# Kernel optimization log

Measured on AMD Instinct MI355X. Metric: run time of the kernel, lower is better.

Reference implementation:

```python
import jax, jax.numpy as jnp
import numpy as np

N_NODES = 50000
N_EDGES = 800000
IN_DIM = 512
HIDDEN = 512
HEADS = 4                       # num_heads // 2 per direction
C_HEAD = HIDDEN // (2 * HEADS)  # 64 -> each direction outputs HIDDEN//2
NEG_SLOPE = 0.2                 # PyG GATConv default leaky_relu slope
BN_EPS = 1e-5


def gat_conv(x, src, dst, W, att_src, att_dst, bias):
    """PyG-style GATConv, concat=True. Edge (src -> dst), aggregated at dst.
    x:[N,D] W:[D,H,C] att_*:[H,C] bias:[H*C] -> [N,H*C]."""
    N = x.shape[0]
    h = jnp.einsum('nd,dhc->nhc', x, W)              # [N,H,C]
    a_s = jnp.sum(h * att_src, axis=-1)              # [N,H]
    a_d = jnp.sum(h * att_dst, axis=-1)              # [N,H]
    e = jax.nn.leaky_relu(a_s[src] + a_d[dst], NEG_SLOPE)   # [E,H]
    m = jax.ops.segment_max(e, dst, num_segments=N)         # [N,H]
    m = jnp.where(jnp.isfinite(m), m, 0.0)
    ex = jnp.exp(e - m[dst])                                # [E,H]
    denom = jax.ops.segment_sum(ex, dst, num_segments=N)    # [N,H]
    alpha = ex / (denom[dst] + 1e-16)                       # [E,H]
    out = jax.ops.segment_sum(alpha[:, :, None] * h[src], dst, num_segments=N)
    return out.reshape(N, HEADS * C_HEAD) + bias


def setup_inputs() -> dict:
    key = jax.random.key(0)
    ks = jax.random.split(key, 12)
    glorot = lambda k, shape, fan: (jax.random.normal(k, shape, jnp.float32)
                                    * np.sqrt(2.0 / fan))
    inp = {
        'x': jax.random.normal(ks[0], (N_NODES, IN_DIM), jnp.float32),
        'edge_index': jax.random.randint(ks[1], (2, N_EDGES), 0, N_NODES,
                                         dtype=jnp.int32).astype(jnp.int64),
        # forward-direction GATConv params
        'W_f': glorot(ks[2], (IN_DIM, HEADS, C_HEAD), IN_DIM),
        'att_src_f': glorot(ks[3], (HEADS, C_HEAD), C_HEAD),
        'att_dst_f': glorot(ks[4], (HEADS, C_HEAD), C_HEAD),
        'bias_f': jnp.zeros((HEADS * C_HEAD,), jnp.float32),
        # backward-direction GATConv params
        'W_b': glorot(ks[5], (IN_DIM, HEADS, C_HEAD), IN_DIM),
        'att_src_b': glorot(ks[6], (HEADS, C_HEAD), C_HEAD),
        'att_dst_b': glorot(ks[7], (HEADS, C_HEAD), C_HEAD),
        'bias_b': jnp.zeros((HEADS * C_HEAD,), jnp.float32),
        # fusion linear + batchnorm
        'W_fuse': glorot(ks[8], (HIDDEN, HIDDEN), HIDDEN),
        'b_fuse': jnp.zeros((HIDDEN,), jnp.float32),
        'bn_gamma': jnp.ones((HIDDEN,), jnp.float32),
        'bn_beta': jnp.zeros((HIDDEN,), jnp.float32),
    }
    return inp


def reference(x, edge_index, W_f, att_src_f, att_dst_f, bias_f,
              W_b, att_src_b, att_dst_b, bias_b,
              W_fuse, b_fuse, bn_gamma, bn_beta):
    src, dst = edge_index[0], edge_index[1]
    fwd = gat_conv(x, src, dst, W_f, att_src_f, att_dst_f, bias_f)
    # reversed edges: torch.flip(edge_index, [0]) swaps src/dst rows
    bwd = gat_conv(x, dst, src, W_b, att_src_b, att_dst_b, bias_b)
    combined = jnp.concatenate([fwd, bwd], axis=1)          # [N, HIDDEN]
    fused = combined @ W_fuse + b_fuse
    mean = jnp.mean(fused, axis=0)
    var = jnp.mean(jnp.square(fused - mean), axis=0)        # biased, as BN uses
    normed = (fused - mean) * jax.lax.rsqrt(var + BN_EPS) * bn_gamma + bn_beta
    return jax.nn.relu(normed)
```

## Files before the change

### kernel.cpp

```cpp
#include <hip/hip_runtime.h>
#include <math.h>

#define HEADS 4
#define CH 64
#define HC 256
#define HID 512
#define KDIM 512

typedef __attribute__((ext_vector_type(8))) short short8;
typedef __attribute__((ext_vector_type(4))) float f32x4;

__device__ __forceinline__ float lrelu(float x){ return x > 0.f ? x : 0.2f*x; }

__device__ __forceinline__ unsigned short f2bf(float f){
  unsigned u = __float_as_uint(f);
  unsigned r = (u + 0x7FFFu + ((u >> 16) & 1u)) >> 16;
  return (unsigned short)r;
}
__device__ __forceinline__ float bf2f(unsigned short u){
  return __uint_as_float(((unsigned)u) << 16);
}

__global__ void k_zero(int* cntD, int* cntS, float* gsum, float* gsq, int N){
  int i = blockIdx.x*blockDim.x + threadIdx.x;
  int stride = gridDim.x*blockDim.x;
  for(int j=i; j<N; j+=stride){ cntD[j]=0; cntS[j]=0; }
  if(i < HID){ gsum[i]=0.f; gsq[i]=0.f; }
}

__global__ void k_detect(const int* __restrict__ ei32, int* flag){
  __shared__ int any;
  if(threadIdx.x==0) any = 0;
  __syncthreads();
  int v = 0;
  for(int i=threadIdx.x; i<1024; i+=blockDim.x) v |= ei32[2*i+1];
  if(v) atomicOr(&any, 1);
  __syncthreads();
  if(threadIdx.x==0) *flag = (any==0) ? 1 : 0;
}

__global__ void k_convert(const int* __restrict__ ei32, const int* __restrict__ flag,
                          int* __restrict__ src, int* __restrict__ dst, int E){
  int i = blockIdx.x*blockDim.x + threadIdx.x;
  if(i>=E) return;
  if(*flag){ src[i] = ei32[2*i];  dst[i] = ei32[2*(E+i)]; }
  else     { src[i] = ei32[i];    dst[i] = ei32[E+i];     }
}

__global__ void k_cvt_x(const float4* __restrict__ in4, uint2* __restrict__ out2, long n4){
  long i = (long)blockIdx.x*blockDim.x + threadIdx.x;
  long stride = (long)gridDim.x*blockDim.x;
  for(long j=i; j<n4; j+=stride){
    float4 v = in4[j];
    uint2 o;
    o.x = (unsigned)f2bf(v.x) | ((unsigned)f2bf(v.y) << 16);
    o.y = (unsigned)f2bf(v.z) | ((unsigned)f2bf(v.w) << 16);
    out2[j] = o;
  }
}

__global__ void k_transcvt(const float* __restrict__ src, unsigned short* __restrict__ dst,
                           int K, int C){
  int i = blockIdx.x*blockDim.x + threadIdx.x;
  if(i >= C*K) return;
  int n = i / K;
  int k = i - n*K;
  dst[(size_t)n*K + k] = f2bf(src[(size_t)k*C + n]);
}

__global__ __launch_bounds__(256) void k_gemm_mfma(
    const unsigned short* __restrict__ A,
    const unsigned short* __restrict__ Bt,
    float* __restrict__ Cf, unsigned short* __restrict__ Cb,
    int M, int Nc, int K, const float* __restrict__ bias){
  __shared__ __align__(16) unsigned short Asm[128*32];
  __shared__ __align__(16) unsigned short Bsm[128*32];
  int tid = threadIdx.x;
  int w = tid >> 6, lane = tid & 63;
  int wr = (w >> 1) * 64, wc = (w & 1) * 64;
  int lcol = lane & 15, lkb = lane >> 4;
  int row0 = blockIdx.y * 128, col0 = blockIdx.x * 128;

  int c0 = tid, c1 = tid + 256;
  int ar0 = c0 >> 2, ak0 = (c0 & 3) * 8;
  int ar1 = c1 >> 2, ak1 = (c1 & 3) * 8;

  f32x4 acc[4][4] = {};

  for(int kt = 0; kt < K; kt += 32){
    short8 va0 = *(const short8*)(A  + (size_t)(row0 + ar0)*K + kt + ak0);
    short8 va1 = *(const short8*)(A  + (size_t)(row0 + ar1)*K + kt + ak1);
    short8 vb0 = *(const short8*)(Bt + (size_t)(col0 + ar0)*K + kt + ak0);
    short8 vb1 = *(const short8*)(Bt + (size_t)(col0 + ar1)*K + kt + ak1);
    __syncthreads();
    *(short8*)(Asm + ar0*32 + ak0) = va0;
    *(short8*)(Asm + ar1*32 + ak1) = va1;
    *(short8*)(Bsm + ar0*32 + ak0) = vb0;
    *(short8*)(Bsm + ar1*32 + ak1) = vb1;
    __syncthreads();

    short8 af[4], bfr[4];
    #pragma unroll
    for(int mi=0; mi<4; mi++)
      af[mi] = *(const short8*)(Asm + (wr + mi*16 + lcol)*32 + lkb*8);
    #pragma unroll
    for(int ni=0; ni<4; ni++)
      bfr[ni] = *(const short8*)(Bsm + (wc + ni*16 + lcol)*32 + lkb*8);
    #pragma unroll
    for(int mi=0; mi<4; mi++)
      #pragma unroll
      for(int ni=0; ni<4; ni++)
        acc[mi][ni] = __builtin_amdgcn_mfma_f32_16x16x32_bf16(af[mi], bfr[ni], acc[mi][ni], 0, 0, 0);
  }

  int lr = (lane >> 4) * 4;
  #pragma unroll
  for(int mi=0; mi<4; mi++){
    int gr0 = row0 + wr + mi*16 + lr;
    #pragma unroll
    for(int ni=0; ni<4; ni++){
      int gc = col0 + wc + ni*16 + lcol;
      float bv = bias ? bias[gc] : 0.f;
      #pragma unroll
      for(int r=0; r<4; r++){
        int gr = gr0 + r;
        if(gr < M){
          float v = acc[mi][ni][r] + bv;
          if(Cb) Cb[(size_t)gr*Nc + gc] = f2bf(v);
          else   Cf[(size_t)gr*Nc + gc] = v;
        }
      }
    }
  }
}

__global__ __launch_bounds__(256) void k_att(
    const unsigned short* __restrict__ h,
    const float* __restrict__ att_sf, const float* __restrict__ att_df,
    const float* __restrict__ att_sb, const float* __restrict__ att_db,
    float4* __restrict__ asf, float4* __restrict__ adf,
    float4* __restrict__ asb, float4* __restrict__ adb, int N){
  int w = (blockIdx.x*(blockDim.x>>6)) + (threadIdx.x>>6);
  int lane = threadIdx.x & 63;
  if(w >= N) return;
  float psf[4], pdf_[4], psb[4], pdb_[4];
  #pragma unroll
  for(int i=0;i<4;i++){
    float vf = bf2f(h[(size_t)w*HID + i*64 + lane]);
    float vb = bf2f(h[(size_t)w*HID + 256 + i*64 + lane]);
    psf[i]  = vf*att_sf[i*64+lane];  pdf_[i] = vf*att_df[i*64+lane];
    psb[i]  = vb*att_sb[i*64+lane];  pdb_[i] = vb*att_db[i*64+lane];
  }
  #pragma unroll
  for(int off=32; off; off>>=1){
    #pragma unroll
    for(int i=0;i<4;i++){
      psf[i]  += __shfl_xor(psf[i],  off);
      pdf_[i] += __shfl_xor(pdf_[i], off);
      psb[i]  += __shfl_xor(psb[i],  off);
      pdb_[i] += __shfl_xor(pdb_[i], off);
    }
  }
  if(lane==0){
    asf[w] = make_float4(psf[0],psf[1],psf[2],psf[3]);
    adf[w] = make_float4(pdf_[0],pdf_[1],pdf_[2],pdf_[3]);
    asb[w] = make_float4(psb[0],psb[1],psb[2],psb[3]);
    adb[w] = make_float4(pdb_[0],pdb_[1],pdb_[2],pdb_[3]);
  }
}

__global__ void k_edge(const int* __restrict__ src, const int* __restrict__ dst,
    const float4* __restrict__ asf, const float4* __restrict__ adf,
    const float4* __restrict__ asb, const float4* __restrict__ adb,
    float4* __restrict__ ef, float4* __restrict__ eb,
    int* __restrict__ cntD, int* __restrict__ cntS, int E){
  int e = blockIdx.x*blockDim.x + threadIdx.x;
  if(e>=E) return;
  int s = src[e], d = dst[e];
  float4 a = asf[s], b = adf[d], r;
  r.x = lrelu(a.x+b.x); r.y = lrelu(a.y+b.y); r.z = lrelu(a.z+b.z); r.w = lrelu(a.w+b.w);
  ef[e] = r;
  a = asb[d]; b = adb[s];
  r.x = lrelu(a.x+b.x); r.y = lrelu(a.y+b.y); r.z = lrelu(a.z+b.z); r.w = lrelu(a.w+b.w);
  eb[e] = r;
  atomicAdd(&cntD[d], 1);
  atomicAdd(&cntS[s], 1);
}

__global__ __launch_bounds__(1024) void k_scan_local(
    const int* __restrict__ cntD, const int* __restrict__ cntS,
    int* __restrict__ rsD, int* __restrict__ curD,
    int* __restrict__ rsS, int* __restrict__ curS,
    int* __restrict__ bsums, int n, int nb){
  const int* cnt = blockIdx.y ? cntS : cntD;
  int* rs  = blockIdx.y ? rsS  : rsD;
  int* cur = blockIdx.y ? curS : curD;
  int* bs  = bsums + blockIdx.y*nb;
  __shared__ int sh[1024];
  int i = blockIdx.x*1024 + threadIdx.x;
  int v = (i<n) ? cnt[i] : 0;
  sh[threadIdx.x] = v;
  __syncthreads();
  for(int off=1; off<1024; off<<=1){
    int t = (threadIdx.x>=off) ? sh[threadIdx.x-off] : 0;
    __syncthreads();
    sh[threadIdx.x] += t;
    __syncthreads();
  }
  if(i<n){ int e0 = sh[threadIdx.x] - v; rs[i] = e0; cur[i] = e0; }
  if(threadIdx.x==1023) bs[blockIdx.x] = sh[1023];
}

__global__ __launch_bounds__(256) void k_scan_bsums(int* __restrict__ bsums,
                                                    int* __restrict__ totals, int nb){
  int* bs = bsums + blockIdx.x*nb;
  __shared__ int sh[256];
  int v = (threadIdx.x < nb) ? bs[threadIdx.x] : 0;
  sh[threadIdx.x] = v;
  __syncthreads();
  for(int off=1; off<256; off<<=1){
    int t = (threadIdx.x>=off) ? sh[threadIdx.x-off] : 0;
    __syncthreads();
    sh[threadIdx.x] += t;
    __syncthreads();
  }
  if(threadIdx.x < nb) bs[threadIdx.x] = sh[threadIdx.x] - v;
  if(threadIdx.x == 255) totals[blockIdx.x] = sh[255];
}

__global__ __launch_bounds__(1024) void k_scan_add(
    int* __restrict__ rsD, int* __restrict__ curD,
    int* __restrict__ rsS, int* __restrict__ curS,
    const int* __restrict__ bsums, const int* __restrict__ totals, int n, int nb){
  const int* bs = bsums + blockIdx.y*nb;
  int* rs  = blockIdx.y ? rsS  : rsD;
  int* cur = blockIdx.y ? curS : curD;
  int add = bs[blockIdx.x];
  int i = blockIdx.x*1024 + threadIdx.x;
  if(i<n){ rs[i] += add; cur[i] += add; }
  if(i==0) rs[n] = totals[blockIdx.y];
}

__global__ void k_scatter(const int* __restrict__ src, const int* __restrict__ dst,
    int* __restrict__ curD, int* __restrict__ curS,
    int* __restrict__ listD, int* __restrict__ listS, int E){
  int e = blockIdx.x*blockDim.x + threadIdx.x;
  if(e>=E) return;
  int p = atomicAdd(&curD[dst[e]], 1);  listD[p] = e;
  int q = atomicAdd(&curS[src[e]], 1);  listS[q] = e;
}

__global__ __launch_bounds__(256) void k_agg(
    const int* __restrict__ rs, const int* __restrict__ list,
    const float4* __restrict__ etab, const int* __restrict__ gidx,
    const unsigned short* __restrict__ h, int hoff, const float* __restrict__ bias,
    unsigned short* __restrict__ combined, int N, int out_off){
  int w = (blockIdx.x*(blockDim.x>>6)) + (threadIdx.x>>6);
  int lane = threadIdx.x & 63;
  if(w >= N) return;
  int beg = rs[w], end = rs[w+1];
  float4 m = make_float4(-1e30f,-1e30f,-1e30f,-1e30f);
  for(int j=beg+lane; j<end; j+=64){
    float4 ev = etab[list[j]];
    m.x = fmaxf(m.x, ev.x); m.y = fmaxf(m.y, ev.y);
    m.z = fmaxf(m.z, ev.z); m.w = fmaxf(m.w, ev.w);
  }
  #pragma unroll
  for(int off=32; off; off>>=1){
    m.x = fmaxf(m.x, __shfl_xor(m.x, off));
    m.y = fmaxf(m.y, __shfl_xor(m.y, off));
    m.z = fmaxf(m.z, __shfl_xor(m.z, off));
    m.w = fmaxf(m.w, __shfl_xor(m.w, off));
  }
  float4 acc = make_float4(0,0,0,0);
  float4 den = make_float4(0,0,0,0);
  for(int j=beg; j<end; j++){
    int e = list[j];
    float4 ev = etab[e];
    int g = gidx[e];
    const unsigned short* hp = h + (size_t)g*HID + hoff;
    float e0 = __expf(ev.x - m.x), e1 = __expf(ev.y - m.y);
    float e2 = __expf(ev.z - m.z), e3 = __expf(ev.w - m.w);
    den.x += e0; den.y += e1; den.z += e2; den.w += e3;
    acc.x += e0 * bf2f(hp[lane]);
    acc.y += e1 * bf2f(hp[64+lane]);
    acc.z += e2 * bf2f(hp[128+lane]);
    acc.w += e3 * bf2f(hp[192+lane]);
  }
  unsigned short* co = combined + (size_t)w*HID + out_off;
  co[lane]     = f2bf(acc.x/(den.x+1e-16f) + bias[lane]);
  co[64+lane]  = f2bf(acc.y/(den.y+1e-16f) + bias[64+lane]);
  co[128+lane] = f2bf(acc.z/(den.z+1e-16f) + bias[128+lane]);
  co[192+lane] = f2bf(acc.w/(den.w+1e-16f) + bias[192+lane]);
}

__global__ __launch_bounds__(512) void k_bn_stats(const unsigned short* __restrict__ fused, int N,
                                                  float* __restrict__ gsum, float* __restrict__ gsq){
  int c = threadIdx.x;
  int rows_per = (N + gridDim.x - 1) / gridDim.x;
  int r0 = blockIdx.x * rows_per;
  int r1 = min(N, r0 + rows_per);
  float s = 0.f, q = 0.f;
  for(int r=r0; r<r1; r++){
    float v = bf2f(fused[(size_t)r*HID + c]);
    s += v; q += v*v;
  }
  atomicAdd(&gsum[c], s);
  atomicAdd(&gsq[c], q);
}

__global__ __launch_bounds__(512) void k_bn_final(const float* __restrict__ gsum, const float* __restrict__ gsq,
    const float* __restrict__ gamma, const float* __restrict__ beta,
    float* __restrict__ scale, float* __restrict__ shift, int N){
  int c = threadIdx.x;
  float mean = gsum[c] / (float)N;
  float var  = gsq[c] / (float)N - mean*mean;
  float sc = gamma[c] * rsqrtf(var + 1e-5f);
  scale[c] = sc;
  shift[c] = beta[c] - mean*sc;
}

__global__ void k_bn_apply(const uint2* __restrict__ fused2, const float4* __restrict__ scale4,
                           const float4* __restrict__ shift4, float4* __restrict__ out4, long n4){
  long i = (long)blockIdx.x*blockDim.x + threadIdx.x;
  long stride = (long)gridDim.x*blockDim.x;
  for(long j=i; j<n4; j+=stride){
    uint2 u = fused2[j];
    int c4 = (int)(j & 127);
    float4 sc = scale4[c4], sh = shift4[c4];
    float4 r;
    r.x = fmaxf(__uint_as_float(u.x << 16)          * sc.x + sh.x, 0.f);
    r.y = fmaxf(__uint_as_float(u.x & 0xffff0000u)  * sc.y + sh.y, 0.f);
    r.z = fmaxf(__uint_as_float(u.y << 16)          * sc.z + sh.z, 0.f);
    r.w = fmaxf(__uint_as_float(u.y & 0xffff0000u)  * sc.w + sh.w, 0.f);
    out4[j] = r;
  }
}

extern "C" void kernel_launch(void* const* d_in, const int* in_sizes, int n_in,
                              void* d_out, int out_size, void* d_ws, size_t ws_size,
                              hipStream_t stream){
  const float* x        = (const float*)d_in[0];
  const int*   ei32     = (const int*)  d_in[1];
  const float* W_f      = (const float*)d_in[2];
  const float* att_sf   = (const float*)d_in[3];
  const float* att_df   = (const float*)d_in[4];
  const float* bias_f   = (const float*)d_in[5];
  const float* W_b      = (const float*)d_in[6];
  const float* att_sb   = (const float*)d_in[7];
  const float* att_db   = (const float*)d_in[8];
  const float* bias_b   = (const float*)d_in[9];
  const float* W_fuse   = (const float*)d_in[10];
  const float* b_fuse   = (const float*)d_in[11];
  const float* bn_gamma = (const float*)d_in[12];
  const float* bn_beta  = (const float*)d_in[13];

  const int N = in_sizes[0] / 512;
  const int E = in_sizes[1] / 2;
  const int Mp = ((N + 127) / 128) * 128;
  const int nb = (N + 1023) / 1024;

  char* ws = (char*)d_ws;
  size_t off = 0;
  auto alloc = [&](size_t bytes)->char*{
    char* p = ws + off;
    off = (off + bytes + 255) & ~(size_t)255;
    return p;
  };

  int*   srcI   = (int*)  alloc((size_t)E*4);
  int*   dstI   = (int*)  alloc((size_t)E*4);
  unsigned short* xb      = (unsigned short*)alloc((size_t)Mp*KDIM*2);
  unsigned short* Wcat_t  = (unsigned short*)alloc((size_t)HID*KDIM*2);
  unsigned short* Wfuse_t = (unsigned short*)alloc((size_t)HID*KDIM*2);
  unsigned short* h       = (unsigned short*)alloc((size_t)Mp*HID*2);
  float4* asf   = (float4*)alloc((size_t)N*16);
  float4* adf   = (float4*)alloc((size_t)N*16);
  float4* asb   = (float4*)alloc((size_t)N*16);
  float4* adb   = (float4*)alloc((size_t)N*16);
  float4* e_f   = (float4*)alloc((size_t)E*16);
  float4* e_b   = (float4*)alloc((size_t)E*16);
  int*   rsD    = (int*)  alloc((size_t)(N+1)*4);
  int*   curD   = (int*)  alloc((size_t)N*4);
  int*   listD  = (int*)  alloc((size_t)E*4);
  int*   rsS    = (int*)  alloc((size_t)(N+1)*4);
  int*   curS   = (int*)  alloc((size_t)N*4);
  int*   listS  = (int*)  alloc((size_t)E*4);
  unsigned short* combined = (unsigned short*)alloc((size_t)Mp*HID*2);
  float* gsum   = (float*)alloc(HID*4);
  float* gsq    = (float*)alloc(HID*4);
  float* scale  = (float*)alloc(HID*4);
  float* shift  = (float*)alloc(HID*4);
  int*   bsums  = (int*)  alloc(2*256*4);
  int*   totals = (int*)  alloc(2*4);
  int*   flag   = (int*)  alloc(4);
  unsigned short* fused = h;

  k_zero<<<256, 256, 0, stream>>>((int*)curD, (int*)curS, gsum, gsq, N);
  k_detect<<<1, 256, 0, stream>>>(ei32, flag);
  k_convert<<<(E+255)/256, 256, 0, stream>>>(ei32, flag, srcI, dstI, E);

  long xn4 = (long)N * KDIM / 4;
  k_cvt_x<<<2048, 256, 0, stream>>>((const float4*)x, (uint2*)xb, xn4);
  k_transcvt<<<(HC*KDIM+255)/256, 256, 0, stream>>>(W_f, Wcat_t, KDIM, HC);
  k_transcvt<<<(HC*KDIM+255)/256, 256, 0, stream>>>(W_b, Wcat_t + (size_t)HC*KDIM, KDIM, HC);
  k_transcvt<<<(HID*KDIM+255)/256, 256, 0, stream>>>(W_fuse, Wfuse_t, KDIM, HID);

  k_gemm_mfma<<<dim3(HID/128, Mp/128), 256, 0, stream>>>(xb, Wcat_t, nullptr, h, N, HID, KDIM, nullptr);

  int nodeBlocks = (N + 3) / 4;
  k_att<<<nodeBlocks, 256, 0, stream>>>(h, att_sf, att_df, att_sb, att_db,
                                        asf, adf, asb, adb, N);

  k_edge<<<(E+255)/256, 256, 0, stream>>>(srcI, dstI, asf, adf, asb, adb,
                                          e_f, e_b, curD, curS, E);

  k_scan_local<<<dim3(nb,2), 1024, 0, stream>>>(curD, curS, rsD, curD, rsS, curS, bsums, N, nb);
  k_scan_bsums<<<2, 256, 0, stream>>>(bsums, totals, nb);
  k_scan_add<<<dim3(nb,2), 1024, 0, stream>>>(rsD, curD, rsS, curS, bsums, totals, N, nb);

  k_scatter<<<(E+255)/256, 256, 0, stream>>>(srcI, dstI, curD, curS, listD, listS, E);

  k_agg<<<nodeBlocks, 256, 0, stream>>>(rsD, listD, e_f, srcI, h, 0,   bias_f, combined, N, 0);
  k_agg<<<nodeBlocks, 256, 0, stream>>>(rsS, listS, e_b, dstI, h, 256, bias_b, combined, N, HC);

  k_gemm_mfma<<<dim3(HID/128, Mp/128), 256, 0, stream>>>(combined, Wfuse_t, nullptr, fused, N, HID, KDIM, b_fuse);

  k_bn_stats<<<128, 512, 0, stream>>>(fused, N, gsum, gsq);
  k_bn_final<<<1, 512, 0, stream>>>(gsum, gsq, bn_gamma, bn_beta, scale, shift, N);
  long n4 = (long)N * HID / 4;
  k_bn_apply<<<2048, 256, 0, stream>>>((const uint2*)fused, (const float4*)scale,
                                       (const float4*)shift, (float4*)d_out, n4);

  (void)n_in; (void)out_size; (void)ws_size;
}
```

Baseline: 1.034 ms.

## Fuse edge-score computation into aggregation and store neighbor ids in CSR lists

Removes the separate edge kernel that materialized per-edge attention logits for both directions and instead recomputes leaky_relu(a_src+a_dst) inside the aggregation from node-level tables. The CSR lists now hold neighbor node ids instead of edge ids, so the extra gather through src/dst is dropped. Degree counting moves into the convert kernel. Both aggregation directions launch as one grid, and each lane handles four contiguous channels of one head with a vectorized bf16 load. The cost is recomputing the logits twice per edge in exchange for saving two E-sized float4 writes and reads.

Result: faster. 943.7 us (-8.7%).

```diff
diff --git a/kernel.cpp b/kernel.cpp
--- a/kernel.cpp
+++ b/kernel.cpp
@@ -40,11 +40,16 @@
 }
 
 __global__ void k_convert(const int* __restrict__ ei32, const int* __restrict__ flag,
-                          int* __restrict__ src, int* __restrict__ dst, int E){
+                          int* __restrict__ src, int* __restrict__ dst,
+                          int* __restrict__ cntD, int* __restrict__ cntS, int E){
   int i = blockIdx.x*blockDim.x + threadIdx.x;
   if(i>=E) return;
-  if(*flag){ src[i] = ei32[2*i];  dst[i] = ei32[2*(E+i)]; }
-  else     { src[i] = ei32[i];    dst[i] = ei32[E+i];     }
+  int s, d;
+  if(*flag){ s = ei32[2*i];  d = ei32[2*(E+i)]; }
+  else     { s = ei32[i];    d = ei32[E+i];     }
+  src[i] = s; dst[i] = d;
+  atomicAdd(&cntD[d], 1);
+  atomicAdd(&cntS[s], 1);
 }
 
 __global__ void k_cvt_x(const float4* __restrict__ in4, uint2* __restrict__ out2, long n4){
@@ -169,24 +174,6 @@
   }
 }
 
-__global__ void k_edge(const int* __restrict__ src, const int* __restrict__ dst,
-    const float4* __restrict__ asf, const float4* __restrict__ adf,
-    const float4* __restrict__ asb, const float4* __restrict__ adb,
-    float4* __restrict__ ef, float4* __restrict__ eb,
-    int* __restrict__ cntD, int* __restrict__ cntS, int E){
-  int e = blockIdx.x*blockDim.x + threadIdx.x;
-  if(e>=E) return;
-  int s = src[e], d = dst[e];
-  float4 a = asf[s], b = adf[d], r;
-  r.x = lrelu(a.x+b.x); r.y = lrelu(a.y+b.y); r.z = lrelu(a.z+b.z); r.w = lrelu(a.w+b.w);
-  ef[e] = r;
-  a = asb[d]; b = adb[s];
-  r.x = lrelu(a.x+b.x); r.y = lrelu(a.y+b.y); r.z = lrelu(a.z+b.z); r.w = lrelu(a.w+b.w);
-  eb[e] = r;
-  atomicAdd(&cntD[d], 1);
-  atomicAdd(&cntS[s], 1);
-}
-
 __global__ __launch_bounds__(1024) void k_scan_local(
     const int* __restrict__ cntD, const int* __restrict__ cntS,
     int* __restrict__ rsD, int* __restrict__ curD,
@@ -246,24 +233,40 @@
     int* __restrict__ listD, int* __restrict__ listS, int E){
   int e = blockIdx.x*blockDim.x + threadIdx.x;
   if(e>=E) return;
-  int p = atomicAdd(&curD[dst[e]], 1);  listD[p] = e;
-  int q = atomicAdd(&curS[src[e]], 1);  listS[q] = e;
-}
-
-__global__ __launch_bounds__(256) void k_agg(
-    const int* __restrict__ rs, const int* __restrict__ list,
-    const float4* __restrict__ etab, const int* __restrict__ gidx,
-    const unsigned short* __restrict__ h, int hoff, const float* __restrict__ bias,
-    unsigned short* __restrict__ combined, int N, int out_off){
-  int w = (blockIdx.x*(blockDim.x>>6)) + (threadIdx.x>>6);
+  int s = src[e], d = dst[e];
+  int p = atomicAdd(&curD[d], 1);  listD[p] = s;
+  int q = atomicAdd(&curS[s], 1);  listS[q] = d;
+}
+
+__global__ __launch_bounds__(256) void k_agg2(
+    const int* __restrict__ rsD, const int* __restrict__ listD,
+    const int* __restrict__ rsS, const int* __restrict__ listS,
+    const float4* __restrict__ asf, const float4* __restrict__ adf,
+    const float4* __restrict__ asb, const float4* __restrict__ adb,
+    const unsigned short* __restrict__ h,
+    const float* __restrict__ bias_f, const float* __restrict__ bias_b,
+    unsigned short* __restrict__ combined, int N){
+  int dir = blockIdx.y;
+  const int* rs     = dir ? rsS   : rsD;
+  const int* list   = dir ? listS : listD;
+  const float4* At  = dir ? asb   : asf;
+  const float4* Bt  = dir ? adb   : adf;
+  const float* bias = dir ? bias_b : bias_f;
+  int off256 = dir ? 256 : 0;
+
+  int w = blockIdx.x*(blockDim.x>>6) + (threadIdx.x>>6);
   int lane = threadIdx.x & 63;
   if(w >= N) return;
   int beg = rs[w], end = rs[w+1];
+  float4 bw = Bt[w];
+
   float4 m = make_float4(-1e30f,-1e30f,-1e30f,-1e30f);
   for(int j=beg+lane; j<end; j+=64){
-    float4 ev = etab[list[j]];
-    m.x = fmaxf(m.x, ev.x); m.y = fmaxf(m.y, ev.y);
-    m.z = fmaxf(m.z, ev.z); m.w = fmaxf(m.w, ev.w);
+    float4 a = At[list[j]];
+    m.x = fmaxf(m.x, lrelu(a.x+bw.x));
+    m.y = fmaxf(m.y, lrelu(a.y+bw.y));
+    m.z = fmaxf(m.z, lrelu(a.z+bw.z));
+    m.w = fmaxf(m.w, lrelu(a.w+bw.w));
   }
   #pragma unroll
   for(int off=32; off; off>>=1){
@@ -272,26 +275,33 @@
     m.z = fmaxf(m.z, __shfl_xor(m.z, off));
     m.w = fmaxf(m.w, __shfl_xor(m.w, off));
   }
-  float4 acc = make_float4(0,0,0,0);
-  float4 den = make_float4(0,0,0,0);
+  int head = lane >> 4;
+  float mh = head==0 ? m.x : head==1 ? m.y : head==2 ? m.z : m.w;
+  float bh = head==0 ? bw.x : head==1 ? bw.y : head==2 ? bw.z : bw.w;
+
+  const float* Atf = (const float*)At;
+  float acc0=0.f, acc1=0.f, acc2=0.f, acc3=0.f, den=0.f;
   for(int j=beg; j<end; j++){
-    int e = list[j];
-    float4 ev = etab[e];
-    int g = gidx[e];
-    const unsigned short* hp = h + (size_t)g*HID + hoff;
-    float e0 = __expf(ev.x - m.x), e1 = __expf(ev.y - m.y);
-    float e2 = __expf(ev.z - m.z), e3 = __expf(ev.w - m.w);
-    den.x += e0; den.y += e1; den.z += e2; den.w += e3;
-    acc.x += e0 * bf2f(hp[lane]);
-    acc.y += e1 * bf2f(hp[64+lane]);
-    acc.z += e2 * bf2f(hp[128+lane]);
-    acc.w += e3 * bf2f(hp[192+lane]);
-  }
-  unsigned short* co = combined + (size_t)w*HID + out_off;
-  co[lane]     = f2bf(acc.x/(den.x+1e-16f) + bias[lane]);
-  co[64+lane]  = f2bf(acc.y/(den.y+1e-16f) + bias[64+lane]);
-  co[128+lane] = f2bf(acc.z/(den.z+1e-16f) + bias[128+lane]);
-  co[192+lane] = f2bf(acc.w/(den.w+1e-16f) + bias[192+lane]);
+    int g = list[j];
+    float ah = Atf[(size_t)g*4 + head];
+    float eh = __expf(lrelu(ah + bh) - mh);
+    den += eh;
+    uint2 u = *(const uint2*)(h + (size_t)g*HID + off256 + lane*4);
+    acc0 += eh * bf2f((unsigned short)(u.x & 0xffffu));
+    acc1 += eh * __uint_as_float(u.x & 0xffff0000u);
+    acc2 += eh * bf2f((unsigned short)(u.y & 0xffffu));
+    acc3 += eh * __uint_as_float(u.y & 0xffff0000u);
+  }
+  float inv = 1.f / (den + 1e-16f);
+  int c = lane*4;
+  float o0 = acc0*inv + bias[c+0];
+  float o1 = acc1*inv + bias[c+1];
+  float o2 = acc2*inv + bias[c+2];
+  float o3 = acc3*inv + bias[c+3];
+  uint2 o;
+  o.x = (unsigned)f2bf(o0) | ((unsigned)f2bf(o1) << 16);
+  o.y = (unsigned)f2bf(o2) | ((unsigned)f2bf(o3) << 16);
+  *(uint2*)(combined + (size_t)w*HID + off256 + c) = o;
 }
 
 __global__ __launch_bounds__(512) void k_bn_stats(const unsigned short* __restrict__ fused, int N,
@@ -378,8 +388,6 @@
   float4* adf   = (float4*)alloc((size_t)N*16);
   float4* asb   = (float4*)alloc((size_t)N*16);
   float4* adb   = (float4*)alloc((size_t)N*16);
-  float4* e_f   = (float4*)alloc((size_t)E*16);
-  float4* e_b   = (float4*)alloc((size_t)E*16);
   int*   rsD    = (int*)  alloc((size_t)(N+1)*4);
   int*   curD   = (int*)  alloc((size_t)N*4);
   int*   listD  = (int*)  alloc((size_t)E*4);
@@ -398,7 +406,7 @@
 
   k_zero<<<256, 256, 0, stream>>>((int*)curD, (int*)curS, gsum, gsq, N);
   k_detect<<<1, 256, 0, stream>>>(ei32, flag);
-  k_convert<<<(E+255)/256, 256, 0, stream>>>(ei32, flag, srcI, dstI, E);
+  k_convert<<<(E+255)/256, 256, 0, stream>>>(ei32, flag, srcI, dstI, curD, curS, E);
 
   long xn4 = (long)N * KDIM / 4;
   k_cvt_x<<<2048, 256, 0, stream>>>((const float4*)x, (uint2*)xb, xn4);
@@ -412,17 +420,15 @@
   k_att<<<nodeBlocks, 256, 0, stream>>>(h, att_sf, att_df, att_sb, att_db,
                                         asf, adf, asb, adb, N);
 
-  k_edge<<<(E+255)/256, 256, 0, stream>>>(srcI, dstI, asf, adf, asb, adb,
-                                          e_f, e_b, curD, curS, E);
-
   k_scan_local<<<dim3(nb,2), 1024, 0, stream>>>(curD, curS, rsD, curD, rsS, curS, bsums, N, nb);
   k_scan_bsums<<<2, 256, 0, stream>>>(bsums, totals, nb);
   k_scan_add<<<dim3(nb,2), 1024, 0, stream>>>(rsD, curD, rsS, curS, bsums, totals, N, nb);
 
   k_scatter<<<(E+255)/256, 256, 0, stream>>>(srcI, dstI, curD, curS, listD, listS, E);
 
-  k_agg<<<nodeBlocks, 256, 0, stream>>>(rsD, listD, e_f, srcI, h, 0,   bias_f, combined, N, 0);
-  k_agg<<<nodeBlocks, 256, 0, stream>>>(rsS, listS, e_b, dstI, h, 256, bias_b, combined, N, HC);
+  k_agg2<<<dim3(nodeBlocks, 2), 256, 0, stream>>>(rsD, listD, rsS, listS,
+                                                  asf, adf, asb, adb, h,
+                                                  bias_f, bias_b, combined, N);
 
   k_gemm_mfma<<<dim3(HID/128, Mp/128), 256, 0, stream>>>(combined, Wfuse_t, nullptr, fused, N, HID, KDIM, b_fuse);
 
```
